# Performance work log

Measured on AMD Instinct MI355X. Metric: run time of the kernel, lower is better.

The kernel has to match this reference:

```python
import jax, jax.numpy as jnp
import numpy as np

B, S, D = 1, 2048, 2048          # batch, context_length, embedding_dimension
H, DH = 16, 128                  # num_heads, head_size (= head_output_dimension)
HID = 4 * D                      # SwiGLU hidden dim
LAMBDA_INIT = 0.8
EPS = 1e-6


def setup_inputs() -> dict:
    key = jax.random.key(0)
    ks = jax.random.split(key, 14)
    nrm = lambda k, sh, s=0.02: jax.random.normal(k, sh, jnp.float32) * s
    return {
        "x": jax.random.normal(ks[0], (B, S, D), jnp.float32),
        "g_norm": jnp.ones((D,), jnp.float32),          # shared RMSNorm gain (same layer used twice)
        "Wq1": nrm(ks[1], (H, D, DH)), "Wq2": nrm(ks[2], (H, D, DH)),
        "Wk1": nrm(ks[3], (H, D, DH)), "Wk2": nrm(ks[4], (H, D, DH)),
        "Wv":  nrm(ks[5], (H, D, DH)),
        "lq1": nrm(ks[6], (H, DH), 0.1), "lk1": nrm(ks[7], (H, DH), 0.1),
        "lq2": nrm(ks[8], (H, DH), 0.1), "lk2": nrm(ks[9], (H, DH), 0.1),
        "Wo": nrm(ks[10], (H * DH, D)),
        "W1": nrm(ks[11], (D, HID)), "W2": nrm(ks[12], (D, HID)), "W3": nrm(ks[13], (HID, D)),
    }


def rmsnorm(x, g):
    return x * jax.lax.rsqrt(jnp.mean(x * x, axis=-1, keepdims=True) + EPS) * g


def diff_attention(x, Wq1, Wq2, Wk1, Wk2, Wv, lq1, lk1, lq2, lk2, Wo):
    # per-head projections: [B,S,D] x [H,D,DH] -> [B,H,S,DH]
    proj = lambda W: jnp.einsum('bsd,hde->bhse', x, W)
    q1, q2 = proj(Wq1), proj(Wq2)
    k1, k2 = proj(Wk1), proj(Wk2)
    v = proj(Wv)
    scale = 1.0 / jnp.sqrt(jnp.float32(DH))
    A1 = jax.nn.softmax(jnp.einsum('bhse,bhte->bhst', q1, k1) * scale, axis=-1)
    A2 = jax.nn.softmax(jnp.einsum('bhse,bhte->bhst', q2, k2) * scale, axis=-1)
    # learned per-head lambda: exp(lq1.lk1) - exp(lq2.lk2) + lambda_init
    lam = (jnp.exp(jnp.sum(lq1 * lk1, -1)) - jnp.exp(jnp.sum(lq2 * lk2, -1)) + LAMBDA_INIT)  # [H]
    o = jnp.einsum('bhst,bhte->bhse', A1 - lam[None, :, None, None] * A2, v)  # [B,H,S,DH]
    o = o.transpose(0, 2, 1, 3).reshape(B, S, H * DH)
    return o @ Wo


def reference(x, g_norm, Wq1, Wq2, Wk1, Wk2, Wv, lq1, lk1, lq2, lk2, Wo, W1, W2, W3):
    # Encoder block (dropout=0 -> identity in eval)
    h = rmsnorm(x, g_norm)
    h = diff_attention(h, Wq1, Wq2, Wk1, Wk2, Wv, lq1, lk1, lq2, lk2, Wo) + h
    z = rmsnorm(h, g_norm)
    ffn = (jax.nn.silu(z @ W1) * (z @ W2)) @ W3  # SwiGLU
    return ffn + h
```

## Files before the change

kernel.cpp:

```cpp
#include <hip/hip_runtime.h>

typedef unsigned short u16;
typedef __bf16 bf16x8 __attribute__((ext_vector_type(8)));
typedef float f32x4 __attribute__((ext_vector_type(4)));

#define S_LEN 2048
#define D_DIM 2048
#define NH 16
#define DH 128
#define HID 8192

__device__ __forceinline__ u16 f2bf(float f) {
  unsigned int u = __float_as_uint(f);
  u += 0x7fff + ((u >> 16) & 1);
  return (u16)(u >> 16);
}

__device__ __forceinline__ void gld16(const u16* g, u16* l) {
  __builtin_amdgcn_global_load_lds(
      (const __attribute__((address_space(1))) unsigned int*)g,
      (__attribute__((address_space(3))) unsigned int*)l, 16, 0, 0);
}

__global__ __launch_bounds__(256) void tconv_f2b(const float* __restrict__ in,
                                                 u16* __restrict__ out, int R, int C) {
  __shared__ float tile[32][33];
  size_t boff = (size_t)blockIdx.z * R * C;
  in += boff; out += boff;
  int c0 = blockIdx.x * 32, r0 = blockIdx.y * 32;
  int tx = threadIdx.x, ty = threadIdx.y;
#pragma unroll
  for (int i = 0; i < 32; i += 8) tile[ty + i][tx] = in[(size_t)(r0 + ty + i) * C + c0 + tx];
  __syncthreads();
#pragma unroll
  for (int i = 0; i < 32; i += 8) out[(size_t)(c0 + ty + i) * R + r0 + tx] = f2bf(tile[tx][ty + i]);
}

__global__ __launch_bounds__(256) void tconv_b2b(const u16* __restrict__ in,
                                                 u16* __restrict__ out, int R, int C) {
  __shared__ u16 tile[32][34];
  size_t boff = (size_t)blockIdx.z * R * C;
  in += boff; out += boff;
  int c0 = blockIdx.x * 32, r0 = blockIdx.y * 32;
  int tx = threadIdx.x, ty = threadIdx.y;
#pragma unroll
  for (int i = 0; i < 32; i += 8) tile[ty + i][tx] = in[(size_t)(r0 + ty + i) * C + c0 + tx];
  __syncthreads();
#pragma unroll
  for (int i = 0; i < 32; i += 8) out[(size_t)(c0 + ty + i) * R + r0 + tx] = tile[tx][ty + i];
}

__global__ __launch_bounds__(256) void rmsnorm_kernel(const float* __restrict__ x,
                                                      const float* __restrict__ g,
                                                      float* __restrict__ xf,
                                                      u16* __restrict__ xb) {
  int row = blockIdx.x;
  int t = threadIdx.x;
  const float4* xr = (const float4*)(x + (size_t)row * D_DIM);
  float4 v0 = xr[t];
  float4 v1 = xr[t + 256];
  float ss = v0.x * v0.x + v0.y * v0.y + v0.z * v0.z + v0.w * v0.w +
             v1.x * v1.x + v1.y * v1.y + v1.z * v1.z + v1.w * v1.w;
#pragma unroll
  for (int o = 1; o < 64; o <<= 1) ss += __shfl_xor(ss, o, 64);
  __shared__ float wss[4];
  if ((t & 63) == 0) wss[t >> 6] = ss;
  __syncthreads();
  float tot = wss[0] + wss[1] + wss[2] + wss[3];
  float rs = rsqrtf(tot * (1.0f / D_DIM) + 1e-6f);
  const float4* gr = (const float4*)g;
  float4 g0 = gr[t], g1 = gr[t + 256];
  float4 o0, o1;
  o0.x = v0.x * rs * g0.x; o0.y = v0.y * rs * g0.y; o0.z = v0.z * rs * g0.z; o0.w = v0.w * rs * g0.w;
  o1.x = v1.x * rs * g1.x; o1.y = v1.y * rs * g1.y; o1.z = v1.z * rs * g1.z; o1.w = v1.w * rs * g1.w;
  if (xf) {
    float4* xfr = (float4*)(xf + (size_t)row * D_DIM);
    xfr[t] = o0; xfr[t + 256] = o1;
  }
  ushort4 b0, b1;
  b0.x = f2bf(o0.x); b0.y = f2bf(o0.y); b0.z = f2bf(o0.z); b0.w = f2bf(o0.w);
  b1.x = f2bf(o1.x); b1.y = f2bf(o1.y); b1.z = f2bf(o1.z); b1.w = f2bf(o1.w);
  ushort4* xbr = (ushort4*)(xb + (size_t)row * D_DIM);
  xbr[t] = b0; xbr[t + 256] = b1;
}

__global__ __launch_bounds__(256) void lam_kernel(const float* __restrict__ lq1,
                                                  const float* __restrict__ lk1,
                                                  const float* __restrict__ lq2,
                                                  const float* __restrict__ lk2,
                                                  float* __restrict__ lamw) {
  int t = threadIdx.x;
  int h = t >> 4, i = (t & 15) << 3;
  float d1 = 0.f, d2 = 0.f;
#pragma unroll
  for (int j = 0; j < 8; j++) {
    d1 += lq1[h * DH + i + j] * lk1[h * DH + i + j];
    d2 += lq2[h * DH + i + j] * lk2[h * DH + i + j];
  }
#pragma unroll
  for (int o = 1; o < 16; o <<= 1) { d1 += __shfl_xor(d1, o, 64); d2 += __shfl_xor(d2, o, 64); }
  if ((t & 15) == 0) lamw[h] = __expf(d1) - __expf(d2) + 0.8f;
}

template <int MODE, int BN>
__global__ __launch_bounds__(256) void gemm_a(const u16* __restrict__ A,
                                              const u16* __restrict__ Bt,
                                              const u16* __restrict__ Bt2,
                                              void* __restrict__ Cout,
                                              const float* __restrict__ res,
                                              int M, int N, int K, long sBt, long sC) {
  constexpr int BM = 128, BK = 32;
  constexpr int JF = BN / 32;
  __shared__ __align__(16) u16 As[BM * BK];
  __shared__ __align__(16) u16 Bs[BN * BK];
  __shared__ __align__(16) u16 Bs2[(MODE == 2) ? BN * BK : 8];
  const int t = threadIdx.x;
  const int lane = t & 63, wid = t >> 6;
  const int wm = (wid >> 1) * 64, wn = (wid & 1) * (BN / 2);
  const int fr = lane & 15, fq = lane >> 4;
  const int m0 = blockIdx.y * BM, n0 = blockIdx.x * BN;
  const u16* bt = Bt + (long)blockIdx.z * sBt;
  f32x4 acc[4][JF] = {};
  f32x4 acc2[(MODE == 2) ? 4 : 1][(MODE == 2) ? JF : 1] = {};
  const int sr = t >> 2, sc = (t & 3) << 3;
  const u16* aG = A + (long)(m0 + sr) * K + sc;
  const u16* bG = bt + (long)(n0 + sr) * K + sc;
  const u16* b2G = (MODE == 2) ? (Bt2 + (long)(n0 + sr) * K + sc) : nullptr;
  u16* aL = &As[t * 8];
  u16* bL = &Bs[t * 8];

  for (int k0 = 0; k0 < K; k0 += BK) {
    __syncthreads();
    gld16(aG + k0, aL);
    gld16(aG + (long)64 * K + k0, aL + 64 * BK);
    gld16(bG + k0, bL);
    if (BN == 128) gld16(bG + (long)64 * K + k0, bL + 64 * BK);
    if (MODE == 2) {
      gld16(b2G + k0, &Bs2[t * 8]);
      if (BN == 128) gld16(b2G + (long)64 * K + k0, &Bs2[t * 8 + 64 * BK]);
    }
    __syncthreads();
    bf16x8 af[4], bfr[JF];
#pragma unroll
    for (int i = 0; i < 4; i++) af[i] = *(const bf16x8*)&As[(wm + i * 16 + fr) * BK + fq * 8];
#pragma unroll
    for (int j = 0; j < JF; j++) bfr[j] = *(const bf16x8*)&Bs[(wn + j * 16 + fr) * BK + fq * 8];
#pragma unroll
    for (int i = 0; i < 4; i++)
#pragma unroll
      for (int j = 0; j < JF; j++)
        acc[i][j] = __builtin_amdgcn_mfma_f32_16x16x32_bf16(af[i], bfr[j], acc[i][j], 0, 0, 0);
    if (MODE == 2) {
      bf16x8 cf[JF];
#pragma unroll
      for (int j = 0; j < JF; j++) cf[j] = *(const bf16x8*)&Bs2[(wn + j * 16 + fr) * BK + fq * 8];
#pragma unroll
      for (int i = 0; i < 4; i++)
#pragma unroll
        for (int j = 0; j < JF; j++)
          acc2[i][j] = __builtin_amdgcn_mfma_f32_16x16x32_bf16(af[i], cf[j], acc2[i][j], 0, 0, 0);
    }
  }

#pragma unroll
  for (int i = 0; i < 4; i++)
#pragma unroll
    for (int j = 0; j < JF; j++) {
      int row0 = m0 + wm + i * 16 + (fq << 2);
      int col = n0 + wn + j * 16 + fr;
#pragma unroll
      for (int r = 0; r < 4; r++) {
        long idx = (long)(row0 + r) * N + col;
        float v = acc[i][j][r];
        if (MODE == 0) {
          ((u16*)Cout + (long)blockIdx.z * sC)[idx] = f2bf(v);
        } else if (MODE == 1) {
          ((float*)Cout)[idx] = v + res[idx];
        } else {
          float g2 = acc2[i][j][r];
          float sg = v / (1.0f + __expf(-v));
          ((u16*)Cout)[idx] = f2bf(sg * g2);
        }
      }
    }
}

#define LDK 136
#define LDV 40
#define LDP 40

__global__ __launch_bounds__(256) void flash_attn(const u16* __restrict__ q1g,
                                                  const u16* __restrict__ q2g,
                                                  const u16* __restrict__ k1g,
                                                  const u16* __restrict__ k2g,
                                                  const u16* __restrict__ vtg,
                                                  const float* __restrict__ lamw,
                                                  u16* __restrict__ og) {
  __shared__ __align__(16) u16 Ks1[32 * LDK];
  __shared__ __align__(16) u16 Ks2[32 * LDK];
  __shared__ __align__(16) u16 Vs[128 * LDV];
  __shared__ __align__(16) u16 Ps[4 * 2 * 16 * LDP];
  const float scale = 0.08838834764831845f;
  int h = blockIdx.y, qt = blockIdx.x;
  size_t hoff = (size_t)h * S_LEN * DH;
  const u16* q1 = q1g + hoff;
  const u16* q2 = q2g + hoff;
  const u16* k1 = k1g + hoff;
  const u16* k2 = k2g + hoff;
  const u16* vt = vtg + hoff;
  int t = threadIdx.x, wid = t >> 6, lane = t & 63;
  int fr = lane & 15, fq = lane >> 4;
  int qrow = qt * 64 + wid * 16 + fr;
  bf16x8 qf1[4], qf2[4];
#pragma unroll
  for (int ks = 0; ks < 4; ks++) {
    qf1[ks] = *(const bf16x8*)&q1[(size_t)qrow * DH + ks * 32 + fq * 8];
    qf2[ks] = *(const bf16x8*)&q2[(size_t)qrow * DH + ks * 32 + fq * 8];
  }
  bf16x8 ones;
#pragma unroll
  for (int i = 0; i < 8; i++) ones[i] = (__bf16)1.0f;

  f32x4 O1[8] = {};
  f32x4 O2[8] = {};
  f32x4 L1 = {};
  f32x4 L2 = {};
  int skr = t >> 3, skc = (t & 7) << 4;
  int svr = t >> 2, svc = (t & 3) << 3;
  u16* myP1 = &Ps[(wid * 2 + 0) * 16 * LDP];
  u16* myP2 = &Ps[(wid * 2 + 1) * 16 * LDP];

  for (int kt = 0; kt < S_LEN; kt += 32) {
    uint4 ka1 = *(const uint4*)&k1[(size_t)(kt + skr) * DH + skc];
    uint4 kb1 = *(const uint4*)&k1[(size_t)(kt + skr) * DH + skc + 8];
    uint4 ka2 = *(const uint4*)&k2[(size_t)(kt + skr) * DH + skc];
    uint4 kb2 = *(const uint4*)&k2[(size_t)(kt + skr) * DH + skc + 8];
    uint4 va = *(const uint4*)&vt[(size_t)svr * S_LEN + kt + svc];
    uint4 vb = *(const uint4*)&vt[(size_t)(svr + 64) * S_LEN + kt + svc];
    __syncthreads();
    *(uint4*)&Ks1[skr * LDK + skc] = ka1;
    *(uint4*)&Ks1[skr * LDK + skc + 8] = kb1;
    *(uint4*)&Ks2[skr * LDK + skc] = ka2;
    *(uint4*)&Ks2[skr * LDK + skc + 8] = kb2;
    *(uint4*)&Vs[svr * LDV + svc] = va;
    *(uint4*)&Vs[(svr + 64) * LDV + svc] = vb;
    __syncthreads();

    f32x4 s1[2] = {};
    f32x4 s2[2] = {};
#pragma unroll
    for (int nf = 0; nf < 2; nf++)
#pragma unroll
      for (int ks = 0; ks < 4; ks++) {
        bf16x8 b1v = *(const bf16x8*)&Ks1[(nf * 16 + fr) * LDK + ks * 32 + fq * 8];
        s1[nf] = __builtin_amdgcn_mfma_f32_16x16x32_bf16(qf1[ks], b1v, s1[nf], 0, 0, 0);
        bf16x8 b2v = *(const bf16x8*)&Ks2[(nf * 16 + fr) * LDK + ks * 32 + fq * 8];
        s2[nf] = __builtin_amdgcn_mfma_f32_16x16x32_bf16(qf2[ks], b2v, s2[nf], 0, 0, 0);
      }

#pragma unroll
    for (int nf = 0; nf < 2; nf++)
#pragma unroll
      for (int r = 0; r < 4; r++) {
        myP1[(fq * 4 + r) * LDP + nf * 16 + fr] = f2bf(__expf(s1[nf][r] * scale));
        myP2[(fq * 4 + r) * LDP + nf * 16 + fr] = f2bf(__expf(s2[nf][r] * scale));
      }
    asm volatile("s_waitcnt lgkmcnt(0)" ::: "memory");
    bf16x8 pa1 = *(const bf16x8*)&myP1[fr * LDP + fq * 8];
    bf16x8 pa2 = *(const bf16x8*)&myP2[fr * LDP + fq * 8];
    L1 = __builtin_amdgcn_mfma_f32_16x16x32_bf16(pa1, ones, L1, 0, 0, 0);
    L2 = __builtin_amdgcn_mfma_f32_16x16x32_bf16(pa2, ones, L2, 0, 0, 0);
#pragma unroll
    for (int f = 0; f < 8; f++) {
      bf16x8 bv = *(const bf16x8*)&Vs[(f * 16 + fr) * LDV + fq * 8];
      O1[f] = __builtin_amdgcn_mfma_f32_16x16x32_bf16(pa1, bv, O1[f], 0, 0, 0);
      O2[f] = __builtin_amdgcn_mfma_f32_16x16x32_bf16(pa2, bv, O2[f], 0, 0, 0);
    }
  }

  float lam = lamw[h];
#pragma unroll
  for (int r = 0; r < 4; r++) {
    float i1 = 1.0f / L1[r], i2 = lam / L2[r];
#pragma unroll
    for (int f = 0; f < 8; f++) {
      float val = O1[f][r] * i1 - O2[f][r] * i2;
      og[(size_t)(qt * 64 + wid * 16 + fq * 4 + r) * (NH * DH) + h * DH + f * 16 + fr] =
          f2bf(val);
    }
  }
}

extern "C" void kernel_launch(void* const* d_in, const int* in_sizes, int n_in,
                              void* d_out, int out_size, void* d_ws, size_t ws_size,
                              hipStream_t stream) {
  const float* x = (const float*)d_in[0];
  const float* g = (const float*)d_in[1];
  const float* Wq1 = (const float*)d_in[2];
  const float* Wq2 = (const float*)d_in[3];
  const float* Wk1 = (const float*)d_in[4];
  const float* Wk2 = (const float*)d_in[5];
  const float* Wv = (const float*)d_in[6];
  const float* lq1 = (const float*)d_in[7];
  const float* lk1 = (const float*)d_in[8];
  const float* lq2 = (const float*)d_in[9];
  const float* lk2 = (const float*)d_in[10];
  const float* Wo = (const float*)d_in[11];
  const float* W1 = (const float*)d_in[12];
  const float* W2 = (const float*)d_in[13];
  const float* W3 = (const float*)d_in[14];

  char* ws = (char*)d_ws;
  size_t off = 0;
  auto alloc = [&](size_t b) {
    char* p = ws + off;
    off += (b + 255) & ~(size_t)255;
    return p;
  };
  const size_t PROJ_B = (size_t)NH * DH * D_DIM * 2;
  u16* wq1t = (u16*)alloc(PROJ_B);
  u16* wq2t = (u16*)alloc(PROJ_B);
  u16* wk1t = (u16*)alloc(PROJ_B);
  u16* wk2t = (u16*)alloc(PROJ_B);
  u16* wvt = (u16*)alloc(PROJ_B);
  u16* wot = (u16*)alloc((size_t)D_DIM * NH * DH * 2);
  u16* w1t = (u16*)alloc((size_t)HID * D_DIM * 2);
  u16* w2t = (u16*)alloc((size_t)HID * D_DIM * 2);
  u16* w3t = (u16*)alloc((size_t)D_DIM * HID * 2);
  u16* xnb = (u16*)alloc((size_t)S_LEN * D_DIM * 2);
  float* xnf = (float*)alloc((size_t)S_LEN * D_DIM * 4);
  u16* q1b = (u16*)alloc(PROJ_B);
  u16* q2b = (u16*)alloc(PROJ_B);
  u16* k1b = (u16*)alloc(PROJ_B);
  u16* k2b = (u16*)alloc(PROJ_B);
  u16* vb = (u16*)alloc(PROJ_B);
  u16* vtb = (u16*)alloc(PROJ_B);
  float* lamw = (float*)alloc(NH * 4);
  u16* oa = (u16*)alloc((size_t)S_LEN * NH * DH * 2);
  float* hf = (float*)alloc((size_t)S_LEN * D_DIM * 4);
  u16* zb = (u16*)alloc((size_t)S_LEN * D_DIM * 2);
  u16* ffb = (u16*)alloc((size_t)S_LEN * HID * 2);
  if (off > ws_size) return;

  dim3 tpb(32, 8);
  tconv_f2b<<<dim3(DH / 32, D_DIM / 32, NH), tpb, 0, stream>>>(Wq1, wq1t, D_DIM, DH);
  tconv_f2b<<<dim3(DH / 32, D_DIM / 32, NH), tpb, 0, stream>>>(Wq2, wq2t, D_DIM, DH);
  tconv_f2b<<<dim3(DH / 32, D_DIM / 32, NH), tpb, 0, stream>>>(Wk1, wk1t, D_DIM, DH);
  tconv_f2b<<<dim3(DH / 32, D_DIM / 32, NH), tpb, 0, stream>>>(Wk2, wk2t, D_DIM, DH);
  tconv_f2b<<<dim3(DH / 32, D_DIM / 32, NH), tpb, 0, stream>>>(Wv, wvt, D_DIM, DH);
  tconv_f2b<<<dim3(D_DIM / 32, (NH * DH) / 32, 1), tpb, 0, stream>>>(Wo, wot, NH * DH, D_DIM);
  tconv_f2b<<<dim3(HID / 32, D_DIM / 32, 1), tpb, 0, stream>>>(W1, w1t, D_DIM, HID);
  tconv_f2b<<<dim3(HID / 32, D_DIM / 32, 1), tpb, 0, stream>>>(W2, w2t, D_DIM, HID);
  tconv_f2b<<<dim3(D_DIM / 32, HID / 32, 1), tpb, 0, stream>>>(W3, w3t, HID, D_DIM);

  rmsnorm_kernel<<<S_LEN, 256, 0, stream>>>(x, g, xnf, xnb);
  lam_kernel<<<1, 256, 0, stream>>>(lq1, lk1, lq2, lk2, lamw);

  long sB = (long)DH * D_DIM, sC = (long)S_LEN * DH;
  gemm_a<0, 128><<<dim3(1, S_LEN / 128, 80), 256, 0, stream>>>(
      xnb, wq1t, nullptr, q1b, nullptr, S_LEN, DH, D_DIM, sB, sC);
  tconv_b2b<<<dim3(DH / 32, S_LEN / 32, NH), tpb, 0, stream>>>(vb, vtb, S_LEN, DH);

  flash_attn<<<dim3(S_LEN / 64, NH), 256, 0, stream>>>(q1b, q2b, k1b, k2b, vtb, lamw, oa);

  gemm_a<1, 64><<<dim3(D_DIM / 64, S_LEN / 128, 1), 256, 0, stream>>>(
      oa, wot, nullptr, hf, xnf, S_LEN, D_DIM, NH * DH, 0, 0);
  rmsnorm_kernel<<<S_LEN, 256, 0, stream>>>(hf, g, nullptr, zb);
  gemm_a<2, 64><<<dim3(HID / 64, S_LEN / 128, 1), 256, 0, stream>>>(
      zb, w1t, w2t, ffb, nullptr, S_LEN, HID, D_DIM, 0, 0);
  gemm_a<1, 64><<<dim3(D_DIM / 64, S_LEN / 128, 1), 256, 0, stream>>>(
      ffb, w3t, nullptr, d_out, hf, S_LEN, D_DIM, HID, 0, 0);
}
```

Before: 989.9 us.

## Double-buffer GEMM LDS tiles, remap blocks across XCDs, raise MFMA priority

The GEMM kernel now keeps two LDS buffers, so the next K tile is loaded asynchronously while MFMAs run on the current one, and each iteration needs one barrier instead of two. Block indices are also remapped so that consecutive logical tiles land on the same XCD, which is meant to improve L2 reuse of shared A/B rows. s_setprio is raised around the MFMA section to favour math issue. The cost is doubled LDS use, which may lower occupancy, and a no-op argument edit to one transpose launch.

```diff
diff --git a/kernel.cpp b/kernel.cpp
--- a/kernel.cpp
+++ b/kernel.cpp
@@ -111,55 +111,81 @@
                                               int M, int N, int K, long sBt, long sC) {
   constexpr int BM = 128, BK = 32;
   constexpr int JF = BN / 32;
-  __shared__ __align__(16) u16 As[BM * BK];
-  __shared__ __align__(16) u16 Bs[BN * BK];
-  __shared__ __align__(16) u16 Bs2[(MODE == 2) ? BN * BK : 8];
+  __shared__ __align__(16) u16 As[2][BM * BK];
+  __shared__ __align__(16) u16 Bs[2][BN * BK];
+  __shared__ __align__(16) u16 Bs2[(MODE == 2) ? 2 : 1][(MODE == 2) ? BN * BK : 8];
   const int t = threadIdx.x;
   const int lane = t & 63, wid = t >> 6;
   const int wm = (wid >> 1) * 64, wn = (wid & 1) * (BN / 2);
   const int fr = lane & 15, fq = lane >> 4;
-  const int m0 = blockIdx.y * BM, n0 = blockIdx.x * BN;
-  const u16* bt = Bt + (long)blockIdx.z * sBt;
+
+  const int gx = gridDim.x, gy = gridDim.y;
+  const int total = gx * gy * (int)gridDim.z;
+  int flat = ((int)blockIdx.z * gy + (int)blockIdx.y) * gx + (int)blockIdx.x;
+  {
+    int q = total >> 3, r = total & 7;
+    int xcd = flat & 7, pos = flat >> 3;
+    flat = ((xcd < r) ? xcd * (q + 1) : r * (q + 1) + (xcd - r) * q) + pos;
+  }
+  const int bz = flat / (gx * gy);
+  const int r2 = flat % (gx * gy);
+  const int by = r2 / gx, bx = r2 % gx;
+
+  const int m0 = by * BM, n0 = bx * BN;
+  const u16* bt = Bt + (long)bz * sBt;
   f32x4 acc[4][JF] = {};
   f32x4 acc2[(MODE == 2) ? 4 : 1][(MODE == 2) ? JF : 1] = {};
   const int sr = t >> 2, sc = (t & 3) << 3;
   const u16* aG = A + (long)(m0 + sr) * K + sc;
   const u16* bG = bt + (long)(n0 + sr) * K + sc;
   const u16* b2G = (MODE == 2) ? (Bt2 + (long)(n0 + sr) * K + sc) : nullptr;
-  u16* aL = &As[t * 8];
-  u16* bL = &Bs[t * 8];
-
+
+  auto stage = [&](int buf, int k0) {
+    gld16(aG + k0, &As[buf][t * 8]);
+    gld16(aG + (long)64 * K + k0, &As[buf][t * 8 + 64 * BK]);
+    gld16(bG + k0, &Bs[buf][t * 8]);
+    if (BN == 128) gld16(bG + (long)64 * K + k0, &Bs[buf][t * 8 + 64 * BK]);
+    if (MODE == 2) {
+      gld16(b2G + k0, &Bs2[buf][t * 8]);
+      if (BN == 128) gld16(b2G + (long)64 * K + k0, &Bs2[buf][t * 8 + 64 * BK]);
+    }
+  };
+
+  stage(0, 0);
+  __syncthreads();
+
+  int cur = 0;
   for (int k0 = 0; k0 < K; k0 += BK) {
-    __syncthreads();
-    gld16(aG + k0, aL);
-    gld16(aG + (long)64 * K + k0, aL + 64 * BK);
-    gld16(bG + k0, bL);
-    if (BN == 128) gld16(bG + (long)64 * K + k0, bL + 64 * BK);
+    if (k0 + BK < K) stage(cur ^ 1, k0 + BK);
+
+    bf16x8 af[4], bfr[JF];
+#pragma unroll
+    for (int i = 0; i < 4; i++) af[i] = *(const bf16x8*)&As[cur][(wm + i * 16 + fr) * BK + fq * 8];
+#pragma unroll
+    for (int j = 0; j < JF; j++) bfr[j] = *(const bf16x8*)&Bs[cur][(wn + j * 16 + fr) * BK + fq * 8];
+    bf16x8 cf[(MODE == 2) ? JF : 1];
     if (MODE == 2) {
-      gld16(b2G + k0, &Bs2[t * 8]);
-      if (BN == 128) gld16(b2G + (long)64 * K + k0, &Bs2[t * 8 + 64 * BK]);
-    }
-    __syncthreads();
-    bf16x8 af[4], bfr[JF];
-#pragma unroll
-    for (int i = 0; i < 4; i++) af[i] = *(const bf16x8*)&As[(wm + i * 16 + fr) * BK + fq * 8];
-#pragma unroll
-    for (int j = 0; j < JF; j++) bfr[j] = *(const bf16x8*)&Bs[(wn + j * 16 + fr) * BK + fq * 8];
+#pragma unroll
+      for (int j = 0; j < JF; j++) cf[j] = *(const bf16x8*)&Bs2[cur][(wn + j * 16 + fr) * BK + fq * 8];
+    }
+
+    __builtin_amdgcn_s_setprio(1);
 #pragma unroll
     for (int i = 0; i < 4; i++)
 #pragma unroll
       for (int j = 0; j < JF; j++)
         acc[i][j] = __builtin_amdgcn_mfma_f32_16x16x32_bf16(af[i], bfr[j], acc[i][j], 0, 0, 0);
     if (MODE == 2) {
-      bf16x8 cf[JF];
-#pragma unroll
-      for (int j = 0; j < JF; j++) cf[j] = *(const bf16x8*)&Bs2[(wn + j * 16 + fr) * BK + fq * 8];
 #pragma unroll
       for (int i = 0; i < 4; i++)
 #pragma unroll
         for (int j = 0; j < JF; j++)
           acc2[i][j] = __builtin_amdgcn_mfma_f32_16x16x32_bf16(af[i], cf[j], acc2[i][j], 0, 0, 0);
     }
+    __builtin_amdgcn_s_setprio(0);
+
+    __syncthreads();
+    cur ^= 1;
   }
 
 #pragma unroll
@@ -173,7 +199,7 @@
         long idx = (long)(row0 + r) * N + col;
         float v = acc[i][j][r];
         if (MODE == 0) {
-          ((u16*)Cout + (long)blockIdx.z * sC)[idx] = f2bf(v);
+          ((u16*)Cout + (long)bz * sC)[idx] = f2bf(v);
         } else if (MODE == 1) {
           ((float*)Cout)[idx] = v + res[idx];
         } else {
@@ -346,7 +372,7 @@
   tconv_f2b<<<dim3(DH / 32, D_DIM / 32, NH), tpb, 0, stream>>>(Wq1, wq1t, D_DIM, DH);
   tconv_f2b<<<dim3(DH / 32, D_DIM / 32, NH), tpb, 0, stream>>>(Wq2, wq2t, D_DIM, DH);
   tconv_f2b<<<dim3(DH / 32, D_DIM / 32, NH), tpb, 0, stream>>>(Wk1, wk1t, D_DIM, DH);
-  tconv_f2b<<<dim3(DH / 32, D_DIM / 32, NH), tpb, 0, stream>>>(Wk2, wk2t, D_DIM, DH);
+  tconv_f2b<<<dim3(DH / 32, D_DIM / 32, NH), tpb, 0, stream>>>(Wk2, wk2t, D_DIM, NH == 16 ? DH : DH);
   tconv_f2b<<<dim3(DH / 32, D_DIM / 32, NH), tpb, 0, stream>>>(Wv, wvt, D_DIM, DH);
   tconv_f2b<<<dim3(D_DIM / 32, (NH * DH) / 32, 1), tpb, 0, stream>>>(Wo, wot, NH * DH, D_DIM);
   tconv_f2b<<<dim3(HID / 32, D_DIM / 32, 1), tpb, 0, stream>>>(W1, w1t, D_DIM, HID);
```

After: 978.9 us. Within noise of the previous version (-1.1%).

## Rewrite GEMM with triple-buffered LDS pipeline, swizzle, and 128x128 tiles

Applied to the files above, without the earlier changes.

Replaces the single-buffered GEMM with a triple-buffered version. Global-to-LDS loads for tile k+2 are issued while tile k is computed, using explicit vmcnt waits and a single barrier per iteration. The kernel also XOR-swizzles the LDS column layout to reduce bank conflicts, widens N tiles to 128 for all GEMMs, raises MFMA priority with s_setprio, and sets occupancy hints in launch_bounds. In exchange it uses more LDS per block and more accumulator registers, which may limit occupancy, and the MODE 0 path now relies on a flat per-head output indexing.

```diff
diff --git a/kernel.cpp b/kernel.cpp
--- a/kernel.cpp
+++ b/kernel.cpp
@@ -102,87 +102,128 @@
   if ((t & 15) == 0) lamw[h] = __expf(d1) - __expf(d2) + 0.8f;
 }
 
-template <int MODE, int BN>
-__global__ __launch_bounds__(256) void gemm_a(const u16* __restrict__ A,
-                                              const u16* __restrict__ Bt,
-                                              const u16* __restrict__ Bt2,
-                                              void* __restrict__ Cout,
-                                              const float* __restrict__ res,
-                                              int M, int N, int K, long sBt, long sC) {
-  constexpr int BM = 128, BK = 32;
-  constexpr int JF = BN / 32;
-  __shared__ __align__(16) u16 As[BM * BK];
-  __shared__ __align__(16) u16 Bs[BN * BK];
-  __shared__ __align__(16) u16 Bs2[(MODE == 2) ? BN * BK : 8];
+template <int MODE>
+__global__ __launch_bounds__(256, (MODE == 2) ? 2 : 3)
+void gemm9(const u16* __restrict__ A, const u16* __restrict__ Bt,
+           const u16* __restrict__ Bt2, void* __restrict__ Cout,
+           const float* __restrict__ res, int N, int K) {
+  __shared__ __align__(16) u16 As[3][128 * 32];
+  __shared__ __align__(16) u16 Bs[3][128 * 32];
+  __shared__ __align__(16) u16 Bs2[(MODE == 2) ? 3 : 1][(MODE == 2) ? 128 * 32 : 8];
   const int t = threadIdx.x;
   const int lane = t & 63, wid = t >> 6;
-  const int wm = (wid >> 1) * 64, wn = (wid & 1) * (BN / 2);
+  const int wm = (wid >> 1) * 64, wn = (wid & 1) * 64;
   const int fr = lane & 15, fq = lane >> 4;
-  const int m0 = blockIdx.y * BM, n0 = blockIdx.x * BN;
-  const u16* bt = Bt + (long)blockIdx.z * sBt;
-  f32x4 acc[4][JF] = {};
-  f32x4 acc2[(MODE == 2) ? 4 : 1][(MODE == 2) ? JF : 1] = {};
-  const int sr = t >> 2, sc = (t & 3) << 3;
-  const u16* aG = A + (long)(m0 + sr) * K + sc;
-  const u16* bG = bt + (long)(n0 + sr) * K + sc;
-  const u16* b2G = (MODE == 2) ? (Bt2 + (long)(n0 + sr) * K + sc) : nullptr;
-  u16* aL = &As[t * 8];
-  u16* bL = &Bs[t * 8];
-
-  for (int k0 = 0; k0 < K; k0 += BK) {
-    __syncthreads();
-    gld16(aG + k0, aL);
-    gld16(aG + (long)64 * K + k0, aL + 64 * BK);
-    gld16(bG + k0, bL);
-    if (BN == 128) gld16(bG + (long)64 * K + k0, bL + 64 * BK);
-    if (MODE == 2) {
-      gld16(b2G + k0, &Bs2[t * 8]);
-      if (BN == 128) gld16(b2G + (long)64 * K + k0, &Bs2[t * 8 + 64 * BK]);
-    }
-    __syncthreads();
-    bf16x8 af[4], bfr[JF];
-#pragma unroll
-    for (int i = 0; i < 4; i++) af[i] = *(const bf16x8*)&As[(wm + i * 16 + fr) * BK + fq * 8];
-#pragma unroll
-    for (int j = 0; j < JF; j++) bfr[j] = *(const bf16x8*)&Bs[(wn + j * 16 + fr) * BK + fq * 8];
-#pragma unroll
-    for (int i = 0; i < 4; i++)
-#pragma unroll
-      for (int j = 0; j < JF; j++)
+  const int m0 = blockIdx.y * 128, n0 = blockIdx.x * 128;
+
+  f32x4 acc[4][4] = {};
+  f32x4 acc2[(MODE == 2) ? 4 : 1][(MODE == 2) ? 4 : 1] = {};
+
+  const int sro = t >> 2;
+  const int scol = ((t & 3) ^ (sro & 3)) << 3;
+  const u16* aSrc = A + (size_t)(m0 + sro) * K + scol;
+  const u16* bSrc = Bt + (size_t)(n0 + sro) * K + scol;
+  const u16* b2Src = (MODE == 2) ? (Bt2 + (size_t)(n0 + sro) * K + scol) : nullptr;
+  const int NT = K >> 5;
+
+  auto stage = [&](int buf, int kof) {
+    gld16(aSrc + kof, &As[buf][t * 8]);
+    gld16(aSrc + (size_t)64 * K + kof, &As[buf][2048 + t * 8]);
+    gld16(bSrc + kof, &Bs[buf][t * 8]);
+    gld16(bSrc + (size_t)64 * K + kof, &Bs[buf][2048 + t * 8]);
+    if constexpr (MODE == 2) {
+      gld16(b2Src + kof, &Bs2[buf][t * 8]);
+      gld16(b2Src + (size_t)64 * K + kof, &Bs2[buf][2048 + t * 8]);
+    }
+  };
+
+  stage(0, 0);
+  stage(1, 32);
+  if constexpr (MODE == 2) asm volatile("s_waitcnt vmcnt(6)" ::: "memory");
+  else                     asm volatile("s_waitcnt vmcnt(4)" ::: "memory");
+  __builtin_amdgcn_s_barrier();
+
+  const int coff = ((fq << 4) ^ ((fr & 3) << 4)) >> 1;
+
+  for (int k = 0; k < NT; ++k) {
+    const int r = k % 3, pbuf = (k + 2) % 3;
+    const bool pf = (k + 2) < NT;
+
+    bf16x8 af[4], bfr[4];
+    bf16x8 b2fr[(MODE == 2) ? 4 : 1];
+#pragma unroll
+    for (int i = 0; i < 4; ++i)
+      af[i] = *(const bf16x8*)&As[r][(wm + i * 16 + fr) * 32 + coff];
+#pragma unroll
+    for (int j = 0; j < 4; ++j)
+      bfr[j] = *(const bf16x8*)&Bs[r][(wn + j * 16 + fr) * 32 + coff];
+    if constexpr (MODE == 2) {
+#pragma unroll
+      for (int j = 0; j < 4; ++j)
+        b2fr[j] = *(const bf16x8*)&Bs2[r][(wn + j * 16 + fr) * 32 + coff];
+    }
+
+    if (pf) stage(pbuf, (k + 2) << 5);
+
+    __builtin_amdgcn_s_setprio(1);
+#pragma unroll
+    for (int i = 0; i < 4; ++i)
+#pragma unroll
+      for (int j = 0; j < 4; ++j)
         acc[i][j] = __builtin_amdgcn_mfma_f32_16x16x32_bf16(af[i], bfr[j], acc[i][j], 0, 0, 0);
-    if (MODE == 2) {
-      bf16x8 cf[JF];
-#pragma unroll
-      for (int j = 0; j < JF; j++) cf[j] = *(const bf16x8*)&Bs2[(wn + j * 16 + fr) * BK + fq * 8];
-#pragma unroll
-      for (int i = 0; i < 4; i++)
-#pragma unroll
-        for (int j = 0; j < JF; j++)
-          acc2[i][j] = __builtin_amdgcn_mfma_f32_16x16x32_bf16(af[i], cf[j], acc2[i][j], 0, 0, 0);
-    }
-  }
-
-#pragma unroll
-  for (int i = 0; i < 4; i++)
-#pragma unroll
-    for (int j = 0; j < JF; j++) {
-      int row0 = m0 + wm + i * 16 + (fq << 2);
-      int col = n0 + wn + j * 16 + fr;
-#pragma unroll
-      for (int r = 0; r < 4; r++) {
-        long idx = (long)(row0 + r) * N + col;
-        float v = acc[i][j][r];
-        if (MODE == 0) {
-          ((u16*)Cout + (long)blockIdx.z * sC)[idx] = f2bf(v);
-        } else if (MODE == 1) {
-          ((float*)Cout)[idx] = v + res[idx];
-        } else {
-          float g2 = acc2[i][j][r];
-          float sg = v / (1.0f + __expf(-v));
-          ((u16*)Cout)[idx] = f2bf(sg * g2);
+    if constexpr (MODE == 2) {
+#pragma unroll
+      for (int i = 0; i < 4; ++i)
+#pragma unroll
+        for (int j = 0; j < 4; ++j)
+          acc2[i][j] = __builtin_amdgcn_mfma_f32_16x16x32_bf16(af[i], b2fr[j], acc2[i][j], 0, 0, 0);
+    }
+    __builtin_amdgcn_s_setprio(0);
+
+    if (k + 1 < NT) {
+      if (pf) {
+        if constexpr (MODE == 2) asm volatile("s_waitcnt vmcnt(6)" ::: "memory");
+        else                     asm volatile("s_waitcnt vmcnt(4)" ::: "memory");
+      } else {
+        asm volatile("s_waitcnt vmcnt(0)" ::: "memory");
+      }
+      __builtin_amdgcn_s_barrier();
+    }
+  }
+
+  if constexpr (MODE == 0) {
+    const size_t headBase = (size_t)(n0 >> 7) * ((size_t)S_LEN * 128);
+#pragma unroll
+    for (int i = 0; i < 4; ++i)
+#pragma unroll
+      for (int j = 0; j < 4; ++j) {
+        int row0 = wm + i * 16 + (fq << 2) + m0;
+        int colL = wn + j * 16 + fr;
+#pragma unroll
+        for (int rr = 0; rr < 4; ++rr)
+          ((u16*)Cout)[headBase + (size_t)(row0 + rr) * 128 + colL] = f2bf(acc[i][j][rr]);
+      }
+  } else {
+#pragma unroll
+    for (int i = 0; i < 4; ++i)
+#pragma unroll
+      for (int j = 0; j < 4; ++j) {
+        int row0 = m0 + wm + i * 16 + (fq << 2);
+        int col = n0 + wn + j * 16 + fr;
+#pragma unroll
+        for (int rr = 0; rr < 4; ++rr) {
+          size_t idx = (size_t)(row0 + rr) * N + col;
+          float v = acc[i][j][rr];
+          if constexpr (MODE == 1) {
+            ((float*)Cout)[idx] = v + res[idx];
+          } else {
+            float g2 = acc2[i][j][rr];
+            float sg = v / (1.0f + __expf(-v));
+            ((u16*)Cout)[idx] = f2bf(sg * g2);
+          }
         }
       }
-    }
+  }
 }
 
 #define LDK 136
@@ -356,18 +397,17 @@
   rmsnorm_kernel<<<S_LEN, 256, 0, stream>>>(x, g, xnf, xnb);
   lam_kernel<<<1, 256, 0, stream>>>(lq1, lk1, lq2, lk2, lamw);
 
-  long sB = (long)DH * D_DIM, sC = (long)S_LEN * DH;
-  gemm_a<0, 128><<<dim3(1, S_LEN / 128, 80), 256, 0, stream>>>(
-      xnb, wq1t, nullptr, q1b, nullptr, S_LEN, DH, D_DIM, sB, sC);
+  gemm9<0><<<dim3((5 * NH * DH) / 128, S_LEN / 128), 256, 0, stream>>>(
+      xnb, wq1t, nullptr, q1b, nullptr, 5 * NH * DH, D_DIM);
   tconv_b2b<<<dim3(DH / 32, S_LEN / 32, NH), tpb, 0, stream>>>(vb, vtb, S_LEN, DH);
 
   flash_attn<<<dim3(S_LEN / 64, NH), 256, 0, stream>>>(q1b, q2b, k1b, k2b, vtb, lamw, oa);
 
-  gemm_a<1, 64><<<dim3(D_DIM / 64, S_LEN / 128, 1), 256, 0, stream>>>(
-      oa, wot, nullptr, hf, xnf, S_LEN, D_DIM, NH * DH, 0, 0);
+  gemm9<1><<<dim3(D_DIM / 128, S_LEN / 128), 256, 0, stream>>>(
+      oa, wot, nullptr, hf, xnf, D_DIM, NH * DH);
   rmsnorm_kernel<<<S_LEN, 256, 0, stream>>>(hf, g, nullptr, zb);
-  gemm_a<2, 64><<<dim3(HID / 64, S_LEN / 128, 1), 256, 0, stream>>>(
-      zb, w1t, w2t, ffb, nullptr, S_LEN, HID, D_DIM, 0, 0);
-  gemm_a<1, 64><<<dim3(D_DIM / 64, S_LEN / 128, 1), 256, 0, stream>>>(
-      ffb, w3t, nullptr, d_out, hf, S_LEN, D_DIM, HID, 0, 0);
-}
+  gemm9<2><<<dim3(HID / 128, S_LEN / 128), 256, 0, stream>>>(
+      zb, w1t, w2t, ffb, nullptr, HID, D_DIM);
+  gemm9<1><<<dim3(D_DIM / 128, S_LEN / 128), 256, 0, stream>>>(
+      ffb, w3t, nullptr, d_out, hf, D_DIM, HID);
+}
```

Result: faster. 888.0 us (-10.3%).
